# Kernel tuning notes

Hardware: AMD Instinct MI355X
Metric: run time of the kernel (lower is better)

## Reference

```python
import jax, jax.numpy as jnp
import numpy as np
from jax import lax

NUM_L2 = 9
# hierarchical validity table: level1 pred 0 -> classes 0..3, pred 1 -> classes 4..8
_VALID = np.full((2, NUM_L2), -np.inf, dtype=np.float32)
_VALID[0, 0:4] = 0.0
_VALID[1, 4:9] = 0.0
MASK_TABLE = jnp.asarray(_VALID)


def setup_inputs() -> dict:
    key = jax.random.key(0)
    ks = jax.random.split(key, 8)
    B, C, H, W = 64, 18, 224, 224
    x = jax.random.normal(ks[0], (B, C, H, W), dtype=jnp.float32)
    model1_pred = jax.random.normal(ks[1], (B, 2), dtype=jnp.float32)
    conv_w = jax.random.normal(ks[2], (32, 18, 3, 3), dtype=jnp.float32) * 0.05
    conv_b = jax.random.normal(ks[3], (32,), dtype=jnp.float32) * 0.05
    fc1_w = jax.random.normal(ks[4], (64, 34), dtype=jnp.float32) * 0.05
    fc1_b = jax.random.normal(ks[5], (64,), dtype=jnp.float32) * 0.05
    fc2_w = jax.random.normal(ks[6], (NUM_L2, 64), dtype=jnp.float32) * 0.05
    fc2_b = jax.random.normal(ks[7], (NUM_L2,), dtype=jnp.float32) * 0.05
    return {"x": x, "model1_pred": model1_pred, "conv_w": conv_w, "conv_b": conv_b,
            "fc1_w": fc1_w, "fc1_b": fc1_b, "fc2_w": fc2_w, "fc2_b": fc2_b}


def reference(x, model1_pred, conv_w, conv_b, fc1_w, fc1_b, fc2_w, fc2_b):
    # conv 18->32, k3, pad 1 (SAME), NCHW
    h = lax.conv_general_dilated(
        x, conv_w, window_strides=(1, 1), padding='SAME',
        dimension_numbers=('NCHW', 'OIHW', 'NCHW'))
    h = jax.nn.relu(h + conv_b[None, :, None, None])
    g = h.mean(axis=(2, 3))                          # [B, 32] global average pool
    f = jnp.concatenate([g, model1_pred], axis=1)    # [B, 34]
    f = jax.nn.relu(f @ fc1_w.T + fc1_b)             # [B, 64]
    logits = f @ fc2_w.T + fc2_b                     # [B, 9]
    idx = jnp.argmax(model1_pred, axis=1)            # [B] level-1 prediction
    mask = MASK_TABLE[idx]                           # gather instead of host loop
    return jax.nn.softmax(logits + mask, axis=1)
```

## Files before the change

### kernel.cpp

```cpp
#include <hip/hip_runtime.h>
#include <math.h>

typedef _Float16 f16;
typedef _Float16 f16x2 __attribute__((ext_vector_type(2)));
typedef _Float16 f16x8 __attribute__((ext_vector_type(8)));
typedef float f32x16 __attribute__((ext_vector_type(16)));

#define BATCH 64
#define IC 18
#define OC 32
#define H 224
#define W 224
#define RSTRIP 28
#define NSTRIP 8
#define NITER (RSTRIP + 2)
#define RECS 226
#define RECW 24
#define SLABF (RECS * RECW)
#define BSTRIDE 72
#define NUM_L2 9

#define MF(a_, b_, c_) c_ = __builtin_amdgcn_mfma_f32_32x32x16_f16((a_), (b_), (c_), 0, 0, 0)

__global__ __launch_bounds__(448, 2)
void conv_mfma_kernel(const float* __restrict__ x,
                      const float* __restrict__ conv_w,
                      const float* __restrict__ conv_b,
                      float* __restrict__ gsum) {
    __shared__ __align__(16) f16 slab[2][SLABF];
    __shared__ __align__(16) f16 Bw[3 * 32 * BSTRIDE];

    const int tid = threadIdx.x;
    const int l   = tid & 63;
    const int wv  = tid >> 6;
    const int lm  = l & 31;
    const int lh  = l >> 5;
    const int b     = blockIdx.x >> 3;
    const int strip = blockIdx.x & 7;
    const int r0    = strip * RSTRIP;

    const int c = tid >> 1;
    const int h = tid & 1;
    const size_t plane = (size_t)H * W;
    const float* xb = x + ((size_t)b * IC + 8 * h) * plane + c;

    for (int idx = tid; idx < 3 * 32 * 64; idx += 448) {
        const int kh = idx >> 11;
        const int oc = (idx >> 6) & 31;
        const int kp = idx & 63;
        int kw = 0, ic = 0, valid = 1;
        if (kp < 18)      { kw = 0; ic = kp; }
        else if (kp < 20) { kw = 2; ic = 16 + (kp - 18); }
        else if (kp < 24) { valid = 0; }
        else if (kp < 42) { kw = 1; ic = kp - 24; }
        else if (kp < 48) { valid = 0; }
        else              { kw = 2; ic = kp - 48; }
        Bw[(kh * 32 + oc) * BSTRIDE + kp] =
            (f16)(valid ? conv_w[oc * 162 + ic * 9 + kh * 3 + kw] : 0.f);
    }
    for (int i = tid; i < 2 * RECS; i += 448) {
        const int buf = (i >= RECS) ? 1 : 0;
        const int rec = buf ? (i - RECS) : i;
        *reinterpret_cast<float2*>(&slab[buf][rec * RECW + 20]) = make_float2(0.f, 0.f);
    }
    for (int i = tid; i < 2 * 20; i += 448) {
        const int buf = (i >= 20) ? 1 : 0;
        const int k = buf ? (i - 20) : i;
        f16x2 z2; z2[0] = (f16)0.f; z2[1] = (f16)0.f;
        if (k < 9)
            *reinterpret_cast<f16x2*>(&slab[buf][0 * RECW + 2 * k]) = z2;
        else if (k == 9)
            *reinterpret_cast<f16x2*>(&slab[buf][224 * RECW + 18]) = z2;
        else
            *reinterpret_cast<f16x2*>(&slab[buf][225 * RECW + 2 * (k - 10)]) = z2;
    }

    auto STAGE_LOAD = [&](int grow, float* sv) {
        const bool inr = (grow >= 0) && (grow < H);
        if (inr) {
            const float* p = xb + (size_t)grow * W;
            #pragma unroll
            for (int j = 0; j < 8; ++j) sv[j] = p[j * plane];
            if (h) { sv[8] = p[8 * plane]; sv[9] = p[9 * plane]; }
            else   { sv[8] = 0.f; sv[9] = 0.f; }
        } else {
            #pragma unroll
            for (int j = 0; j < 10; ++j) sv[j] = 0.f;
        }
    };
    auto STAGE_WRITE = [&](int buf, const float* sv) {
        f16* sw = &slab[buf][0];
        f16x8 v;
        #pragma unroll
        for (int j = 0; j < 8; ++j) v[j] = (f16)sv[j];
        *reinterpret_cast<f16x8*>(&sw[(c + 1) * RECW + 8 * h]) = v;
        if (h) {
            f16x2 p2; p2[0] = (f16)sv[8]; p2[1] = (f16)sv[9];
            *reinterpret_cast<f16x2*>(&sw[(c + 1) * RECW + 16]) = p2;
            f16x2 pp = p2;
            if (c == 0) { pp[0] = (f16)0.f; pp[1] = (f16)0.f; }
            const int prec = (c == 0) ? 223 : (c - 1);
            *reinterpret_cast<f16x2*>(&sw[prec * RECW + 18]) = pp;
        }
    };

    {
        float sv[10];
        STAGE_LOAD(r0 - 1, sv);
        STAGE_WRITE(0, sv);
    }
    __syncthreads();

    f16x8 bfr[3][4];
    #pragma unroll
    for (int kh = 0; kh < 3; ++kh)
        #pragma unroll
        for (int cc = 0; cc < 4; ++cc)
            bfr[kh][cc] = *reinterpret_cast<const f16x8*>(
                &Bw[(kh * 32 + lm) * BSTRIDE + 16 * cc + 8 * lh]);

    const float bias = conv_b[lm];
    float pacc = 0.f;
    f32x16 acc0, acc1, acc2;
    #pragma unroll
    for (int i = 0; i < 16; ++i) { acc0[i] = 0.f; acc1[i] = 0.f; acc2[i] = 0.f; }

    const int abase = RECW * (32 * wv + lm) + 8 * lh;

    auto ITER = [&](int gi, f32x16& aK0, f32x16& aK1, f32x16& aK2) {
        const int cur = gi & 1;
        const bool do_stage = (gi != NITER - 1);
        float sv[10];
        if (do_stage) STAGE_LOAD(r0 + gi, sv);

        const f16* sb = &slab[cur][0];
        const f16x8 a0 = *reinterpret_cast<const f16x8*>(&sb[abase]);
        const f16x8 a1 = *reinterpret_cast<const f16x8*>(&sb[abase + 16]);
        const f16x8 a2 = *reinterpret_cast<const f16x8*>(&sb[abase + 32]);
        const f16x8 a3 = *reinterpret_cast<const f16x8*>(&sb[abase + 48]);
        MF(a0, bfr[0][0], aK0); MF(a1, bfr[0][1], aK0); MF(a2, bfr[0][2], aK0); MF(a3, bfr[0][3], aK0);
        MF(a0, bfr[1][0], aK1); MF(a1, bfr[1][1], aK1); MF(a2, bfr[1][2], aK1); MF(a3, bfr[1][3], aK1);
        MF(a0, bfr[2][0], aK2); MF(a1, bfr[2][1], aK2); MF(a2, bfr[2][2], aK2); MF(a3, bfr[2][3], aK2);

        if (gi >= 2) {
            float s = 0.f;
            #pragma unroll
            for (int i = 0; i < 16; ++i) s += fmaxf(aK2[i] + bias, 0.f);
            pacc += s;
        }
        #pragma unroll
        for (int i = 0; i < 16; ++i) aK2[i] = 0.f;

        if (do_stage) STAGE_WRITE(cur ^ 1, sv);
        __syncthreads();
    };

    for (int g3 = 0; g3 < NITER; g3 += 3) {
        ITER(g3 + 0, acc2, acc1, acc0);
        ITER(g3 + 1, acc0, acc2, acc1);
        ITER(g3 + 2, acc1, acc0, acc2);
    }

    pacc += __shfl_xor(pacc, 32);
    if (l < 32) atomicAdd(&gsum[b * OC + lm], pacc);
}

__global__ void head_kernel(const float* __restrict__ gsum,
                            const float* __restrict__ pred,
                            const float* __restrict__ fc1_w,
                            const float* __restrict__ fc1_b,
                            const float* __restrict__ fc2_w,
                            const float* __restrict__ fc2_b,
                            float* __restrict__ out) {
    const int b = threadIdx.x;
    if (b >= BATCH) return;

    float feat[34];
    const float inv = 1.f / (float)(H * W);
    #pragma unroll
    for (int c = 0; c < 32; ++c) feat[c] = gsum[b * 32 + c] * inv;
    feat[32] = pred[b * 2 + 0];
    feat[33] = pred[b * 2 + 1];

    float f[64];
    for (int j = 0; j < 64; ++j) {
        float s = fc1_b[j];
        #pragma unroll
        for (int k = 0; k < 34; ++k) s += feat[k] * fc1_w[j * 34 + k];
        f[j] = fmaxf(s, 0.f);
    }

    float lg[NUM_L2];
    for (int c = 0; c < NUM_L2; ++c) {
        float s = fc2_b[c];
        #pragma unroll
        for (int j = 0; j < 64; ++j) s += f[j] * fc2_w[c * 64 + j];
        lg[c] = s;
    }

    const int idx = (pred[b * 2 + 1] > pred[b * 2 + 0]) ? 1 : 0;
    const int lo = idx ? 4 : 0;
    const int hi = idx ? 9 : 4;

    float m = -1e30f;
    for (int c = lo; c < hi; ++c) m = fmaxf(m, lg[c]);
    float e[NUM_L2];
    float ssum = 0.f;
    for (int c = 0; c < NUM_L2; ++c) {
        const float v = (c >= lo && c < hi) ? expf(lg[c] - m) : 0.f;
        e[c] = v;
        ssum += v;
    }
    const float rs = 1.f / ssum;
    for (int c = 0; c < NUM_L2; ++c) out[b * NUM_L2 + c] = e[c] * rs;
}

extern "C" void kernel_launch(void* const* d_in, const int* in_sizes, int n_in,
                              void* d_out, int out_size, void* d_ws, size_t ws_size,
                              hipStream_t stream) {
    const float* x      = (const float*)d_in[0];
    const float* pred   = (const float*)d_in[1];
    const float* conv_w = (const float*)d_in[2];
    const float* conv_b = (const float*)d_in[3];
    const float* fc1_w  = (const float*)d_in[4];
    const float* fc1_b  = (const float*)d_in[5];
    const float* fc2_w  = (const float*)d_in[6];
    const float* fc2_b  = (const float*)d_in[7];
    float* out  = (float*)d_out;
    float* gsum = (float*)d_ws;

    hipMemsetAsync(gsum, 0, BATCH * OC * sizeof(float), stream);
    conv_mfma_kernel<<<BATCH * NSTRIP, 448, 0, stream>>>(x, conv_w, conv_b, gsum);
    head_kernel<<<1, 64, 0, stream>>>(gsum, pred, fc1_w, fc1_b, fc2_w, fc2_b, out);
}
```

Measured before the change: 412.6 us.

## Decompose conv into independent per-wave 32-column tiles with private ring buffers

The conv work is split so that each wave owns its own 32x28 output tile and keeps a private 4-slot ring of input rows in LDS. This removes block-wide __syncthreads from the row loop and the three-accumulator rotation. Atomics are replaced by per-tile partial sums that the head kernel reduces, and the head is now parallelised with one block per batch element. The cost is redundant halo loads for tile edges, extra lanes that load the two edge columns, and more blocks with smaller LDS footprints.

```diff
diff --git a/kernel.cpp b/kernel.cpp
--- a/kernel.cpp
+++ b/kernel.cpp
@@ -13,21 +13,25 @@
 #define W 224
 #define RSTRIP 28
 #define NSTRIP 8
-#define NITER (RSTRIP + 2)
-#define RECS 226
+#define NTILE 7
+#define WPB 4
+#define KPW (NTILE * NSTRIP)
+#define UNITS (BATCH * KPW)
+#define NBLOCK (UNITS / WPB)
+#define RECS 34
 #define RECW 24
-#define SLABF (RECS * RECW)
+#define SLOTF (RECS * RECW)
 #define BSTRIDE 72
 #define NUM_L2 9
 
 #define MF(a_, b_, c_) c_ = __builtin_amdgcn_mfma_f32_32x32x16_f16((a_), (b_), (c_), 0, 0, 0)
 
-__global__ __launch_bounds__(448, 2)
+__global__ __launch_bounds__(256, 4)
 void conv_mfma_kernel(const float* __restrict__ x,
                       const float* __restrict__ conv_w,
                       const float* __restrict__ conv_b,
-                      float* __restrict__ gsum) {
-    __shared__ __align__(16) f16 slab[2][SLABF];
+                      float* __restrict__ part) {
+    __shared__ __align__(16) f16 slab[WPB][4][SLOTF];
     __shared__ __align__(16) f16 Bw[3 * 32 * BSTRIDE];
 
     const int tid = threadIdx.x;
@@ -35,16 +39,16 @@
     const int wv  = tid >> 6;
     const int lm  = l & 31;
     const int lh  = l >> 5;
-    const int b     = blockIdx.x >> 3;
-    const int strip = blockIdx.x & 7;
-    const int r0    = strip * RSTRIP;
-
-    const int c = tid >> 1;
-    const int h = tid & 1;
-    const size_t plane = (size_t)H * W;
-    const float* xb = x + ((size_t)b * IC + 8 * h) * plane + c;
-
-    for (int idx = tid; idx < 3 * 32 * 64; idx += 448) {
+
+    const int unit = blockIdx.x * WPB + wv;
+    const int b    = unit / KPW;
+    const int rem  = unit - b * KPW;
+    const int t    = rem % NTILE;
+    const int s    = rem / NTILE;
+    const int r0   = s * RSTRIP;
+    const int col0 = t * 32 - 1;
+
+    for (int idx = tid; idx < 3 * 32 * 64; idx += 256) {
         const int kh = idx >> 11;
         const int oc = (idx >> 6) & 31;
         const int kp = idx & 63;
@@ -58,58 +62,84 @@
         Bw[(kh * 32 + oc) * BSTRIDE + kp] =
             (f16)(valid ? conv_w[oc * 162 + ic * 9 + kh * 3 + kw] : 0.f);
     }
-    for (int i = tid; i < 2 * RECS; i += 448) {
-        const int buf = (i >= RECS) ? 1 : 0;
-        const int rec = buf ? (i - RECS) : i;
-        *reinterpret_cast<float2*>(&slab[buf][rec * RECW + 20]) = make_float2(0.f, 0.f);
-    }
-    for (int i = tid; i < 2 * 20; i += 448) {
-        const int buf = (i >= 20) ? 1 : 0;
-        const int k = buf ? (i - 20) : i;
+
+    for (int i = l; i < 4 * RECS; i += 64) {
+        const int sl  = i / RECS;
+        const int rec = i - sl * RECS;
+        f16* q = &slab[wv][sl][rec * RECW];
         f16x2 z2; z2[0] = (f16)0.f; z2[1] = (f16)0.f;
-        if (k < 9)
-            *reinterpret_cast<f16x2*>(&slab[buf][0 * RECW + 2 * k]) = z2;
-        else if (k == 9)
-            *reinterpret_cast<f16x2*>(&slab[buf][224 * RECW + 18]) = z2;
-        else
-            *reinterpret_cast<f16x2*>(&slab[buf][225 * RECW + 2 * (k - 10)]) = z2;
-    }
-
-    auto STAGE_LOAD = [&](int grow, float* sv) {
-        const bool inr = (grow >= 0) && (grow < H);
-        if (inr) {
-            const float* p = xb + (size_t)grow * W;
+        *reinterpret_cast<f16x2*>(&q[20]) = z2;
+        *reinterpret_cast<f16x2*>(&q[22]) = z2;
+        if (rec >= 32) *reinterpret_cast<f16x2*>(&q[18]) = z2;
+    }
+    __syncthreads();
+
+    const int p   = l >> 1;
+    const int hh  = l & 1;
+    const int col = col0 + p;
+    const bool colok = (col >= 0) & (col < W);
+    const size_t plane = (size_t)H * W;
+    const float* xb = x + ((size_t)b * IC + 8 * hh) * plane + col;
+    const int er   = 32 + (l >> 1);
+    const int ecol = col0 + er;
+    const bool eok = (l < 4) & (ecol < W);
+    const float* xe = x + ((size_t)b * IC + 8 * hh) * plane + ecol;
+
+    auto STAGE_LOAD = [&](int g, float* sv, float* sve) {
+        const bool rok = (g >= 0) & (g < H);
+        if (rok & colok) {
+            const float* q = xb + (size_t)g * W;
             #pragma unroll
-            for (int j = 0; j < 8; ++j) sv[j] = p[j * plane];
-            if (h) { sv[8] = p[8 * plane]; sv[9] = p[9 * plane]; }
-            else   { sv[8] = 0.f; sv[9] = 0.f; }
+            for (int j = 0; j < 8; ++j) sv[j] = q[j * plane];
+            if (hh) { sv[8] = q[8 * plane]; sv[9] = q[9 * plane]; }
+            else    { sv[8] = 0.f; sv[9] = 0.f; }
         } else {
             #pragma unroll
             for (int j = 0; j < 10; ++j) sv[j] = 0.f;
         }
+        if (l < 4) {
+            if (rok & eok) {
+                const float* q = xe + (size_t)g * W;
+                #pragma unroll
+                for (int j = 0; j < 8; ++j) sve[j] = q[j * plane];
+                if (hh) { sve[8] = q[8 * plane]; sve[9] = q[9 * plane]; }
+                else    { sve[8] = 0.f; sve[9] = 0.f; }
+            } else {
+                #pragma unroll
+                for (int j = 0; j < 10; ++j) sve[j] = 0.f;
+            }
+        }
     };
-    auto STAGE_WRITE = [&](int buf, const float* sv) {
-        f16* sw = &slab[buf][0];
+    auto STAGE_WRITE = [&](int slot, const float* sv, const float* sve) {
+        f16* sw = &slab[wv][slot][0];
         f16x8 v;
         #pragma unroll
         for (int j = 0; j < 8; ++j) v[j] = (f16)sv[j];
-        *reinterpret_cast<f16x8*>(&sw[(c + 1) * RECW + 8 * h]) = v;
-        if (h) {
-            f16x2 p2; p2[0] = (f16)sv[8]; p2[1] = (f16)sv[9];
-            *reinterpret_cast<f16x2*>(&sw[(c + 1) * RECW + 16]) = p2;
-            f16x2 pp = p2;
-            if (c == 0) { pp[0] = (f16)0.f; pp[1] = (f16)0.f; }
-            const int prec = (c == 0) ? 223 : (c - 1);
-            *reinterpret_cast<f16x2*>(&sw[prec * RECW + 18]) = pp;
+        *reinterpret_cast<f16x8*>(&sw[p * RECW + 8 * hh]) = v;
+        if (hh) {
+            f16x2 c2; c2[0] = (f16)sv[8]; c2[1] = (f16)sv[9];
+            *reinterpret_cast<f16x2*>(&sw[p * RECW + 16]) = c2;
+            if (p >= 2)
+                *reinterpret_cast<f16x2*>(&sw[(p - 2) * RECW + 18]) = c2;
+        }
+        if (l < 4) {
+            f16x8 w8;
+            #pragma unroll
+            for (int j = 0; j < 8; ++j) w8[j] = (f16)sve[j];
+            *reinterpret_cast<f16x8*>(&sw[er * RECW + 8 * hh]) = w8;
+            if (hh) {
+                f16x2 e2; e2[0] = (f16)sve[8]; e2[1] = (f16)sve[9];
+                *reinterpret_cast<f16x2*>(&sw[er * RECW + 16]) = e2;
+                *reinterpret_cast<f16x2*>(&sw[(er - 2) * RECW + 18]) = e2;
+            }
         }
     };
 
-    {
-        float sv[10];
-        STAGE_LOAD(r0 - 1, sv);
-        STAGE_WRITE(0, sv);
-    }
-    __syncthreads();
+    for (int g = r0 - 1; g <= r0 + 1; ++g) {
+        float sv[10], sve[10];
+        STAGE_LOAD(g, sv, sve);
+        STAGE_WRITE(g & 3, sv, sve);
+    }
 
     f16x8 bfr[3][4];
     #pragma unroll
@@ -121,98 +151,97 @@
 
     const float bias = conv_b[lm];
     float pacc = 0.f;
-    f32x16 acc0, acc1, acc2;
+    f32x16 acc;
     #pragma unroll
-    for (int i = 0; i < 16; ++i) { acc0[i] = 0.f; acc1[i] = 0.f; acc2[i] = 0.f; }
-
-    const int abase = RECW * (32 * wv + lm) + 8 * lh;
-
-    auto ITER = [&](int gi, f32x16& aK0, f32x16& aK1, f32x16& aK2) {
-        const int cur = gi & 1;
-        const bool do_stage = (gi != NITER - 1);
-        float sv[10];
-        if (do_stage) STAGE_LOAD(r0 + gi, sv);
-
-        const f16* sb = &slab[cur][0];
-        const f16x8 a0 = *reinterpret_cast<const f16x8*>(&sb[abase]);
-        const f16x8 a1 = *reinterpret_cast<const f16x8*>(&sb[abase + 16]);
-        const f16x8 a2 = *reinterpret_cast<const f16x8*>(&sb[abase + 32]);
-        const f16x8 a3 = *reinterpret_cast<const f16x8*>(&sb[abase + 48]);
-        MF(a0, bfr[0][0], aK0); MF(a1, bfr[0][1], aK0); MF(a2, bfr[0][2], aK0); MF(a3, bfr[0][3], aK0);
-        MF(a0, bfr[1][0], aK1); MF(a1, bfr[1][1], aK1); MF(a2, bfr[1][2], aK1); MF(a3, bfr[1][3], aK1);
-        MF(a0, bfr[2][0], aK2); MF(a1, bfr[2][1], aK2); MF(a2, bfr[2][2], aK2); MF(a3, bfr[2][3], aK2);
-
-        if (gi >= 2) {
-            float s = 0.f;
-            #pragma unroll
-            for (int i = 0; i < 16; ++i) s += fmaxf(aK2[i] + bias, 0.f);
-            pacc += s;
-        }
-        #pragma unroll
-        for (int i = 0; i < 16; ++i) aK2[i] = 0.f;
-
-        if (do_stage) STAGE_WRITE(cur ^ 1, sv);
-        __syncthreads();
-    };
-
-    for (int g3 = 0; g3 < NITER; g3 += 3) {
-        ITER(g3 + 0, acc2, acc1, acc0);
-        ITER(g3 + 1, acc0, acc2, acc1);
-        ITER(g3 + 2, acc1, acc0, acc2);
+    for (int i = 0; i < 16; ++i) acc[i] = 0.f;
+
+    const int abase = RECW * lm + 8 * lh;
+
+    for (int r = r0; r < r0 + RSTRIP; ++r) {
+        const bool do_stage = (r != r0 + RSTRIP - 1);
+        float sv[10], sve[10];
+        if (do_stage) STAGE_LOAD(r + 2, sv, sve);
+
+        #pragma unroll
+        for (int kh = 0; kh < 3; ++kh) {
+            const f16* sb = &slab[wv][(r - 1 + kh) & 3][0];
+            const f16x8 a0 = *reinterpret_cast<const f16x8*>(&sb[abase]);
+            const f16x8 a1 = *reinterpret_cast<const f16x8*>(&sb[abase + 16]);
+            const f16x8 a2 = *reinterpret_cast<const f16x8*>(&sb[abase + 32]);
+            const f16x8 a3 = *reinterpret_cast<const f16x8*>(&sb[abase + 48]);
+            MF(a0, bfr[kh][0], acc); MF(a1, bfr[kh][1], acc);
+            MF(a2, bfr[kh][2], acc); MF(a3, bfr[kh][3], acc);
+        }
+
+        float ssum = 0.f;
+        #pragma unroll
+        for (int i = 0; i < 16; ++i) ssum += fmaxf(acc[i] + bias, 0.f);
+        pacc += ssum;
+        #pragma unroll
+        for (int i = 0; i < 16; ++i) acc[i] = 0.f;
+
+        if (do_stage) STAGE_WRITE((r + 2) & 3, sv, sve);
     }
 
     pacc += __shfl_xor(pacc, 32);
-    if (l < 32) atomicAdd(&gsum[b * OC + lm], pacc);
+    if (l < 32) part[((size_t)b * KPW + rem) * 32 + lm] = pacc;
 }
 
-__global__ void head_kernel(const float* __restrict__ gsum,
+__global__ void head_kernel(const float* __restrict__ part,
                             const float* __restrict__ pred,
                             const float* __restrict__ fc1_w,
                             const float* __restrict__ fc1_b,
                             const float* __restrict__ fc2_w,
                             const float* __restrict__ fc2_b,
                             float* __restrict__ out) {
-    const int b = threadIdx.x;
-    if (b >= BATCH) return;
-
-    float feat[34];
-    const float inv = 1.f / (float)(H * W);
-    #pragma unroll
-    for (int c = 0; c < 32; ++c) feat[c] = gsum[b * 32 + c] * inv;
-    feat[32] = pred[b * 2 + 0];
-    feat[33] = pred[b * 2 + 1];
-
-    float f[64];
-    for (int j = 0; j < 64; ++j) {
-        float s = fc1_b[j];
-        #pragma unroll
-        for (int k = 0; k < 34; ++k) s += feat[k] * fc1_w[j * 34 + k];
-        f[j] = fmaxf(s, 0.f);
-    }
-
-    float lg[NUM_L2];
-    for (int c = 0; c < NUM_L2; ++c) {
-        float s = fc2_b[c];
-        #pragma unroll
-        for (int j = 0; j < 64; ++j) s += f[j] * fc2_w[c * 64 + j];
-        lg[c] = s;
-    }
-
-    const int idx = (pred[b * 2 + 1] > pred[b * 2 + 0]) ? 1 : 0;
-    const int lo = idx ? 4 : 0;
-    const int hi = idx ? 9 : 4;
-
-    float m = -1e30f;
-    for (int c = lo; c < hi; ++c) m = fmaxf(m, lg[c]);
-    float e[NUM_L2];
-    float ssum = 0.f;
-    for (int c = 0; c < NUM_L2; ++c) {
-        const float v = (c >= lo && c < hi) ? expf(lg[c] - m) : 0.f;
-        e[c] = v;
-        ssum += v;
-    }
-    const float rs = 1.f / ssum;
-    for (int c = 0; c < NUM_L2; ++c) out[b * NUM_L2 + c] = e[c] * rs;
+    __shared__ float feat[34];
+    __shared__ float fsh[64];
+    __shared__ float lsh[NUM_L2];
+    const int b = blockIdx.x;
+    const int tI = threadIdx.x;
+
+    if (tI < 32) {
+        float sres = 0.f;
+        const float* pp = part + (size_t)b * KPW * 32 + tI;
+        for (int k = 0; k < KPW; ++k) sres += pp[k * 32];
+        feat[tI] = sres * (1.f / (float)(H * W));
+    } else if (tI < 34) {
+        feat[tI] = pred[b * 2 + (tI - 32)];
+    }
+    __syncthreads();
+
+    {
+        float sum = fc1_b[tI];
+        #pragma unroll
+        for (int k = 0; k < 34; ++k) sum += feat[k] * fc1_w[tI * 34 + k];
+        fsh[tI] = fmaxf(sum, 0.f);
+    }
+    __syncthreads();
+
+    if (tI < NUM_L2) {
+        float sum = fc2_b[tI];
+        #pragma unroll
+        for (int j = 0; j < 64; ++j) sum += fsh[j] * fc2_w[tI * 64 + j];
+        lsh[tI] = sum;
+    }
+    __syncthreads();
+
+    if (tI == 0) {
+        const int idx = (pred[b * 2 + 1] > pred[b * 2 + 0]) ? 1 : 0;
+        const int lo = idx ? 4 : 0;
+        const int hi = idx ? 9 : 4;
+        float m = -1e30f;
+        for (int c = lo; c < hi; ++c) m = fmaxf(m, lsh[c]);
+        float e[NUM_L2];
+        float ssum = 0.f;
+        for (int c = 0; c < NUM_L2; ++c) {
+            const float v = (c >= lo && c < hi) ? expf(lsh[c] - m) : 0.f;
+            e[c] = v;
+            ssum += v;
+        }
+        const float rs = 1.f / ssum;
+        for (int c = 0; c < NUM_L2; ++c) out[b * NUM_L2 + c] = e[c] * rs;
+    }
 }
 
 extern "C" void kernel_launch(void* const* d_in, const int* in_sizes, int n_in,
@@ -227,9 +256,8 @@
     const float* fc2_w  = (const float*)d_in[6];
     const float* fc2_b  = (const float*)d_in[7];
     float* out  = (float*)d_out;
-    float* gsum = (float*)d_ws;
-
-    hipMemsetAsync(gsum, 0, BATCH * OC * sizeof(float), stream);
-    conv_mfma_kernel<<<BATCH * NSTRIP, 448, 0, stream>>>(x, conv_w, conv_b, gsum);
-    head_kernel<<<1, 64, 0, stream>>>(gsum, pred, fc1_w, fc1_b, fc2_w, fc2_b, out);
+    float* part = (float*)d_ws;
+
+    conv_mfma_kernel<<<NBLOCK, 256, 0, stream>>>(x, conv_w, conv_b, part);
+    head_kernel<<<BATCH, 64, 0, stream>>>(part, pred, fc1_w, fc1_b, fc2_w, fc2_b, out);
 }
```

Result: faster. 365.9 us (-11.3%).
